# Kernel tuning notes

Measured on AMD Instinct MI355X. Metric: run time of the kernel, lower is better.

Reference implementation:

```python
import jax, jax.numpy as jnp
import numpy as np


def setup_inputs() -> dict:
    key = jax.random.key(0)
    ks = jax.random.split(key, 7)
    B, N, K, D = 256, 50, 12, 128
    return {
        "batch_size": B,
        "itm_emb": jax.random.normal(ks[0], (B, N, D), jnp.float32),
        "ave_sess_itms_emb": jax.random.normal(ks[1], (B, N, D), jnp.float32),
        "glob_adj_itm_embs": jax.random.normal(ks[2], (B, N, K, D), jnp.float32),
        "glob_adj_wgt_embs": jax.random.normal(ks[3], (B, N, K), jnp.float32),
        "w1": jax.random.normal(ks[4], (D + 1, D), jnp.float32) * 0.1,
        "w2": jax.random.normal(ks[5], (D, 1), jnp.float32) * 0.1,
        "w3": jax.random.normal(ks[6], (2 * D, D), jnp.float32) * 0.1,
    }


def reference(batch_size, itm_emb, ave_sess_itms_emb, glob_adj_itm_embs,
              glob_adj_wgt_embs, w1, w2, w3):
    D = itm_emb.shape[-1]
    # [B,N,1,D] * [B,N,K,D] -> [B,N,K,D]; concat weight -> [B,N,K,D+1]
    alpha = ave_sess_itms_emb[:, :, None, :] * glob_adj_itm_embs
    alpha = jnp.concatenate([alpha, glob_adj_wgt_embs[..., None]], axis=-1)
    alpha = jnp.einsum('bnkc,cd->bnkd', alpha, w1)          # [B,N,K,D]
    alpha = jax.nn.leaky_relu(alpha, negative_slope=0.2)
    alpha = jnp.einsum('bnkd,do->bnk', alpha, w2)           # [B,N,K]
    alpha = jax.nn.softmax(alpha, axis=-1)[..., None]       # [B,N,K,1]
    att = jnp.sum(alpha * glob_adj_itm_embs, axis=-2)       # [B,N,D]
    g = jnp.concatenate([itm_emb, att], axis=-1)            # [B,N,2D]
    # dropout with p=0.0 / eval mode is identity
    g = jnp.einsum('bnc,cd->bnd', g, w3)
    g = g.reshape(batch_size, -1, D)
    return jax.nn.relu(g)
```

## Files before the change

### kernel.cpp

```cpp
#include <hip/hip_runtime.h>

#define DD 128
#define KADJ 12
#define BN_TOTAL 12800

typedef float f32x4 __attribute__((ext_vector_type(4)));
typedef float f32x2 __attribute__((ext_vector_type(2)));
typedef __bf16 bf16x8 __attribute__((ext_vector_type(8)));
typedef unsigned int u32;

__device__ __forceinline__ bf16x8 cvt8(f32x4 a, f32x4 b) {
    bf16x8 r;
    r[0] = (__bf16)a[0]; r[1] = (__bf16)a[1]; r[2] = (__bf16)a[2]; r[3] = (__bf16)a[3];
    r[4] = (__bf16)b[0]; r[5] = (__bf16)b[1]; r[6] = (__bf16)b[2]; r[7] = (__bf16)b[3];
    return r;
}

__global__ void k_prep(const float* __restrict__ w1, const float* __restrict__ w3,
                       __bf16* __restrict__ w1f, __bf16* __restrict__ w3f) {
    int idx = blockIdx.x * 256 + threadIdx.x;
    int lane = (idx >> 3) & 63, e = idx & 7;
    int l = lane & 15, gg = lane >> 4;
    if (idx < 16384) {
        int fi = idx >> 9, n = fi >> 2, ks = fi & 3;
        int k = ks * 32 + gg * 8 + e;
        w1f[idx] = (__bf16)w1[k * DD + n * 16 + l];
    } else {
        int j = idx - 16384;
        int fi = j >> 9, n = fi >> 3, ks = fi & 7;
        int k = ks * 32 + gg * 8 + e;
        w3f[j] = (__bf16)w3[k * DD + n * 16 + l];
    }
}

__launch_bounds__(256, 4)
__global__ void k_att(const float* __restrict__ ave, const float* __restrict__ adj,
                      const float* __restrict__ wgt, const float* __restrict__ w1,
                      const float* __restrict__ w2, const __bf16* __restrict__ w1f,
                      float* __restrict__ att_out) {
    __shared__ unsigned char lds[32768 + 4 * 3072];
    __bf16* w1s = (__bf16*)lds;
    const int t = threadIdx.x;
    const int lane = t & 63;
    const int w = t >> 6;
    const int l = lane & 15, g = lane >> 4;
    const int bn = blockIdx.x * 4 + w;
    unsigned char* adjb = lds + 32768 + w * 3072;

    {
        const f32x4* src = (const f32x4*)w1f;
        f32x4* dst = (f32x4*)w1s;
        #pragma unroll
        for (int p = 0; p < 8; ++p) dst[p * 256 + t] = src[p * 256 + t];
    }
    __syncthreads();

    const int l2 = l < KADJ ? l : KADJ - 1;
    const float* ar = adj + ((size_t)bn * KADJ + l2) * DD + g * 8;
    const float* er = ave + (size_t)bn * DD + g * 8;
    f32x4 pa[8], pe[8];
    #pragma unroll
    for (int s = 0; s < 4; ++s) {
        pa[2 * s]     = *reinterpret_cast<const f32x4*>(ar + s * 32);
        pa[2 * s + 1] = *reinterpret_cast<const f32x4*>(ar + s * 32 + 4);
        pe[2 * s]     = *reinterpret_cast<const f32x4*>(er + s * 32);
        pe[2 * s + 1] = *reinterpret_cast<const f32x4*>(er + s * 32 + 4);
    }
    f32x4 wv = (g < 3) ? *reinterpret_cast<const f32x4*>(wgt + (size_t)bn * KADJ + g * 4)
                       : f32x4{0.f, 0.f, 0.f, 0.f};

    bf16x8 af[4];
    #pragma unroll
    for (int s = 0; s < 4; ++s) {
        af[s] = cvt8(pa[2 * s] * pe[2 * s], pa[2 * s + 1] * pe[2 * s + 1]);
        if (l < KADJ) {
            int c8 = g + 4 * s;
            *reinterpret_cast<bf16x8*>(adjb + l * 256 + ((c8 ^ l) << 4)) =
                cvt8(pa[2 * s], pa[2 * s + 1]);
        }
    }

    f32x4 acc[8];
    #pragma unroll
    for (int n = 0; n < 8; ++n) acc[n] = f32x4{0.f, 0.f, 0.f, 0.f};
    const __bf16* wb = w1s + lane * 8;
    #pragma unroll
    for (int ks = 0; ks < 4; ++ks)
        #pragma unroll
        for (int n = 0; n < 8; ++n) {
            bf16x8 bq = *reinterpret_cast<const bf16x8*>(wb + (size_t)(n * 4 + ks) * 512);
            acc[n] = __builtin_amdgcn_mfma_f32_16x16x32_bf16(af[ks], bq, acc[n], 0, 0, 0);
        }

    float p[4] = {0.f, 0.f, 0.f, 0.f};
    #pragma unroll
    for (int n = 0; n < 8; ++n) {
        float w1rn = w1[128 * DD + n * 16 + l];
        float w2vn = w2[n * 16 + l];
        #pragma unroll
        for (int j = 0; j < 4; ++j) {
            float h = fmaf(wv[j], w1rn, acc[n][j]);
            h = h > 0.f ? h : 0.2f * h;
            p[j] = fmaf(h, w2vn, p[j]);
        }
    }
    #pragma unroll
    for (int j = 0; j < 4; ++j) {
        p[j] += __shfl_xor(p[j], 1, 64);
        p[j] += __shfl_xor(p[j], 2, 64);
        p[j] += __shfl_xor(p[j], 4, 64);
        p[j] += __shfl_xor(p[j], 8, 64);
        if (g == 3) p[j] = -1e30f;
    }
    float q0[4], q1[4], q2[4];
    #pragma unroll
    for (int j = 0; j < 4; ++j) {
        q0[j] = __shfl_xor(p[j], 16, 64);
        q1[j] = __shfl_xor(p[j], 32, 64);
        q2[j] = __shfl_xor(q1[j], 16, 64);
    }
    float mx = -1e30f;
    #pragma unroll
    for (int j = 0; j < 4; ++j)
        mx = fmaxf(mx, fmaxf(fmaxf(p[j], q0[j]), fmaxf(q1[j], q2[j])));
    float ssum = 0.f;
    #pragma unroll
    for (int j = 0; j < 4; ++j) {
        ssum += __expf(p[j] - mx);  ssum += __expf(q0[j] - mx);
        ssum += __expf(q1[j] - mx); ssum += __expf(q2[j] - mx);
    }
    float inv = 1.f / ssum;

    float a0 = 0.f, a1 = 0.f;
    #pragma unroll
    for (int k = 0; k < KADJ; ++k) {
        int d = (k >> 2) ^ g, j = k & 3;
        float sv = (d == 0) ? p[j] : (d == 1) ? q0[j] : (d == 2) ? q1[j] : q2[j];
        float alpha = __expf(sv - mx) * inv;
        u32 pk = *reinterpret_cast<const u32*>(
            adjb + k * 256 + (((lane >> 2) ^ k) << 4) + (lane & 3) * 4);
        float e0 = __builtin_bit_cast(float, pk << 16);
        float e1 = __builtin_bit_cast(float, pk & 0xFFFF0000u);
        a0 = fmaf(alpha, e0, a0);
        a1 = fmaf(alpha, e1, a1);
    }
    *reinterpret_cast<f32x2*>(att_out + (size_t)bn * DD + lane * 2) = f32x2{a0, a1};
}

__launch_bounds__(256)
__global__ void k_out(const float* __restrict__ itm, const float* att,
                      const __bf16* __restrict__ w3f, float* outp) {
    const int t = threadIdx.x;
    const int lane = t & 63;
    const int w = t >> 6;
    const int l = lane & 15, g = lane >> 4;
    const int R0 = blockIdx.x * 64 + w * 16;
    const int row = R0 + l;

    bf16x8 afr[8];
    const float* ip = itm + (size_t)row * DD;
    #pragma unroll
    for (int s = 0; s < 4; ++s) {
        int c = s * 32 + g * 8;
        f32x4 a0 = *reinterpret_cast<const f32x4*>(ip + c);
        f32x4 a1 = *reinterpret_cast<const f32x4*>(ip + c + 4);
        afr[s] = cvt8(a0, a1);
    }
    const float* ap = att + (size_t)row * DD;
    #pragma unroll
    for (int s = 0; s < 4; ++s) {
        int c = s * 32 + g * 8;
        f32x4 a0 = *reinterpret_cast<const f32x4*>(ap + c);
        f32x4 a1 = *reinterpret_cast<const f32x4*>(ap + c + 4);
        afr[4 + s] = cvt8(a0, a1);
    }

    f32x4 acc[8];
    #pragma unroll
    for (int n = 0; n < 8; ++n) acc[n] = f32x4{0.f, 0.f, 0.f, 0.f};
    #pragma unroll
    for (int s = 0; s < 8; ++s) {
        const __bf16* bp = w3f + ((size_t)s * 64 + lane) * 8;
        #pragma unroll
        for (int n = 0; n < 8; ++n) {
            bf16x8 bfr = *reinterpret_cast<const bf16x8*>(bp + (size_t)n * 4096);
            acc[n] = __builtin_amdgcn_mfma_f32_16x16x32_bf16(afr[s], bfr, acc[n], 0, 0, 0);
        }
    }

    #pragma unroll
    for (int n = 0; n < 8; ++n) {
        #pragma unroll
        for (int j = 0; j < 4; ++j)
            outp[(size_t)(R0 + g * 4 + j) * DD + n * 16 + l] = fmaxf(acc[n][j], 0.f);
    }
}

extern "C" void kernel_launch(void* const* d_in, const int* in_sizes, int n_in,
                              void* d_out, int out_size, void* d_ws, size_t ws_size,
                              hipStream_t stream) {
    const float* itm = (const float*)d_in[1];
    const float* ave = (const float*)d_in[2];
    const float* adj = (const float*)d_in[3];
    const float* wgt = (const float*)d_in[4];
    const float* w1  = (const float*)d_in[5];
    const float* w2  = (const float*)d_in[6];
    const float* w3  = (const float*)d_in[7];
    float* outp = (float*)d_out;

    __bf16* w1f = (__bf16*)d_ws;
    __bf16* w3f = (__bf16*)((char*)d_ws + 32 * 1024);

    k_prep<<<dim3(192), dim3(256), 0, stream>>>(w1, w3, w1f, w3f);
    k_att<<<dim3(BN_TOTAL / 4), dim3(256), 0, stream>>>(ave, adj, wgt, w1, w2, w1f, outp);
    k_out<<<dim3(BN_TOTAL / 64), dim3(256), 0, stream>>>(itm, outp, w3f, outp);
}
```

Baseline: 49.69 us.

## Process two rows per wave in attention kernel, reread adjacency from cache

Each wave in k_att now handles two (b,n) rows instead of one, so the per-block copy of w1 into LDS is shared across twice as many rows. Both rows' adjacency tiles are loaded up front so their memory latency overlaps. The bf16 adjacency staging in LDS is dropped; the weighted sum now reloads fp32 adjacency from global memory, relying on L2 hits and gaining full precision. w2 and the last w1 row are also staged in LDS. The trade-offs are higher register pressure and extra global reloads in exchange for less LDS traffic and fewer blocks.

```diff
diff --git a/kernel.cpp b/kernel.cpp
--- a/kernel.cpp
+++ b/kernel.cpp
@@ -7,7 +7,6 @@
 typedef float f32x4 __attribute__((ext_vector_type(4)));
 typedef float f32x2 __attribute__((ext_vector_type(2)));
 typedef __bf16 bf16x8 __attribute__((ext_vector_type(8)));
-typedef unsigned int u32;
 
 __device__ __forceinline__ bf16x8 cvt8(f32x4 a, f32x4 b) {
     bf16x8 r;
@@ -33,51 +32,19 @@
     }
 }
 
-__launch_bounds__(256, 4)
-__global__ void k_att(const float* __restrict__ ave, const float* __restrict__ adj,
-                      const float* __restrict__ wgt, const float* __restrict__ w1,
-                      const float* __restrict__ w2, const __bf16* __restrict__ w1f,
-                      float* __restrict__ att_out) {
-    __shared__ unsigned char lds[32768 + 4 * 3072];
-    __bf16* w1s = (__bf16*)lds;
-    const int t = threadIdx.x;
-    const int lane = t & 63;
-    const int w = t >> 6;
-    const int l = lane & 15, g = lane >> 4;
-    const int bn = blockIdx.x * 4 + w;
-    unsigned char* adjb = lds + 32768 + w * 3072;
-
-    {
-        const f32x4* src = (const f32x4*)w1f;
-        f32x4* dst = (f32x4*)w1s;
-        #pragma unroll
-        for (int p = 0; p < 8; ++p) dst[p * 256 + t] = src[p * 256 + t];
-    }
-    __syncthreads();
-
-    const int l2 = l < KADJ ? l : KADJ - 1;
-    const float* ar = adj + ((size_t)bn * KADJ + l2) * DD + g * 8;
-    const float* er = ave + (size_t)bn * DD + g * 8;
-    f32x4 pa[8], pe[8];
+__device__ __forceinline__ void process_bn(
+    const f32x4 P[8], f32x4 WG, int BN, int lane, int l, int g,
+    const __bf16* w1s, const float* w2s, const float* w1rs,
+    const float* __restrict__ ave, const float* __restrict__ adj,
+    float* __restrict__ att_out) {
+
+    const float* er = ave + (size_t)BN * DD + g * 8;
+    bf16x8 af[4];
     #pragma unroll
     for (int s = 0; s < 4; ++s) {
-        pa[2 * s]     = *reinterpret_cast<const f32x4*>(ar + s * 32);
-        pa[2 * s + 1] = *reinterpret_cast<const f32x4*>(ar + s * 32 + 4);
-        pe[2 * s]     = *reinterpret_cast<const f32x4*>(er + s * 32);
-        pe[2 * s + 1] = *reinterpret_cast<const f32x4*>(er + s * 32 + 4);
-    }
-    f32x4 wv = (g < 3) ? *reinterpret_cast<const f32x4*>(wgt + (size_t)bn * KADJ + g * 4)
-                       : f32x4{0.f, 0.f, 0.f, 0.f};
-
-    bf16x8 af[4];
-    #pragma unroll
-    for (int s = 0; s < 4; ++s) {
-        af[s] = cvt8(pa[2 * s] * pe[2 * s], pa[2 * s + 1] * pe[2 * s + 1]);
-        if (l < KADJ) {
-            int c8 = g + 4 * s;
-            *reinterpret_cast<bf16x8*>(adjb + l * 256 + ((c8 ^ l) << 4)) =
-                cvt8(pa[2 * s], pa[2 * s + 1]);
-        }
+        f32x4 e0 = *reinterpret_cast<const f32x4*>(er + s * 32);
+        f32x4 e1 = *reinterpret_cast<const f32x4*>(er + s * 32 + 4);
+        af[s] = cvt8(P[2 * s] * e0, P[2 * s + 1] * e1);
     }
 
     f32x4 acc[8];
@@ -95,11 +62,11 @@
     float p[4] = {0.f, 0.f, 0.f, 0.f};
     #pragma unroll
     for (int n = 0; n < 8; ++n) {
-        float w1rn = w1[128 * DD + n * 16 + l];
-        float w2vn = w2[n * 16 + l];
+        float w1rn = w1rs[n * 16 + l];
+        float w2vn = w2s[n * 16 + l];
         #pragma unroll
         for (int j = 0; j < 4; ++j) {
-            float h = fmaf(wv[j], w1rn, acc[n][j]);
+            float h = fmaf(WG[j], w1rn, acc[n][j]);
             h = h > 0.f ? h : 0.2f * h;
             p[j] = fmaf(h, w2vn, p[j]);
         }
@@ -131,20 +98,70 @@
     }
     float inv = 1.f / ssum;
 
+    const float* adjp = adj + (size_t)BN * (KADJ * DD);
     float a0 = 0.f, a1 = 0.f;
     #pragma unroll
     for (int k = 0; k < KADJ; ++k) {
         int d = (k >> 2) ^ g, j = k & 3;
         float sv = (d == 0) ? p[j] : (d == 1) ? q0[j] : (d == 2) ? q1[j] : q2[j];
         float alpha = __expf(sv - mx) * inv;
-        u32 pk = *reinterpret_cast<const u32*>(
-            adjb + k * 256 + (((lane >> 2) ^ k) << 4) + (lane & 3) * 4);
-        float e0 = __builtin_bit_cast(float, pk << 16);
-        float e1 = __builtin_bit_cast(float, pk & 0xFFFF0000u);
-        a0 = fmaf(alpha, e0, a0);
-        a1 = fmaf(alpha, e1, a1);
-    }
-    *reinterpret_cast<f32x2*>(att_out + (size_t)bn * DD + lane * 2) = f32x2{a0, a1};
+        a0 = fmaf(alpha, adjp[k * DD + lane], a0);
+        a1 = fmaf(alpha, adjp[k * DD + 64 + lane], a1);
+    }
+    att_out[(size_t)BN * DD + lane] = a0;
+    att_out[(size_t)BN * DD + 64 + lane] = a1;
+}
+
+__launch_bounds__(256, 4)
+__global__ void k_att(const float* __restrict__ ave, const float* __restrict__ adj,
+                      const float* __restrict__ wgt, const float* __restrict__ w1,
+                      const float* __restrict__ w2, const __bf16* __restrict__ w1f,
+                      float* __restrict__ att_out) {
+    __shared__ __bf16 w1s[16384];
+    __shared__ float w2s[128];
+    __shared__ float w1rs[128];
+
+    const int t = threadIdx.x;
+    const int lane = t & 63;
+    const int w = t >> 6;
+    const int l = lane & 15, g = lane >> 4;
+    const int bn0 = blockIdx.x * 8 + w * 2;
+
+    {
+        const f32x4* src = (const f32x4*)w1f;
+        f32x4* dst = (f32x4*)w1s;
+        #pragma unroll
+        for (int p = 0; p < 8; ++p) dst[p * 256 + t] = src[p * 256 + t];
+        if (t < 128) { w2s[t] = w2[t]; w1rs[t] = w1[128 * DD + t]; }
+    }
+    __syncthreads();
+
+    const int l2 = l < KADJ ? l : KADJ - 1;
+
+    f32x4 paA[8], paB[8], wgA, wgB;
+    {
+        const float* ar = adj + ((size_t)bn0 * KADJ + l2) * DD + g * 8;
+        #pragma unroll
+        for (int s = 0; s < 4; ++s) {
+            paA[2 * s]     = *reinterpret_cast<const f32x4*>(ar + s * 32);
+            paA[2 * s + 1] = *reinterpret_cast<const f32x4*>(ar + s * 32 + 4);
+        }
+        wgA = (g < 3) ? *reinterpret_cast<const f32x4*>(wgt + (size_t)bn0 * KADJ + g * 4)
+                      : f32x4{0.f, 0.f, 0.f, 0.f};
+    }
+    {
+        const float* ar = adj + ((size_t)(bn0 + 1) * KADJ + l2) * DD + g * 8;
+        #pragma unroll
+        for (int s = 0; s < 4; ++s) {
+            paB[2 * s]     = *reinterpret_cast<const f32x4*>(ar + s * 32);
+            paB[2 * s + 1] = *reinterpret_cast<const f32x4*>(ar + s * 32 + 4);
+        }
+        wgB = (g < 3) ? *reinterpret_cast<const f32x4*>(wgt + (size_t)(bn0 + 1) * KADJ + g * 4)
+                      : f32x4{0.f, 0.f, 0.f, 0.f};
+    }
+
+    process_bn(paA, wgA, bn0,     lane, l, g, w1s, w2s, w1rs, ave, adj, att_out);
+    process_bn(paB, wgB, bn0 + 1, lane, l, g, w1s, w2s, w1rs, ave, adj, att_out);
 }
 
 __launch_bounds__(256)
@@ -212,6 +229,6 @@
     __bf16* w3f = (__bf16*)((char*)d_ws + 32 * 1024);
 
     k_prep<<<dim3(192), dim3(256), 0, stream>>>(w1, w3, w1f, w3f);
-    k_att<<<dim3(BN_TOTAL / 4), dim3(256), 0, stream>>>(ave, adj, wgt, w1, w2, w1f, outp);
+    k_att<<<dim3(BN_TOTAL / 8), dim3(256), 0, stream>>>(ave, adj, wgt, w1, w2, w1f, outp);
     k_out<<<dim3(BN_TOTAL / 64), dim3(256), 0, stream>>>(itm, outp, w3f, outp);
 }
```

Measured after the change: 119.9 us. 141% more time.
